# Kernel tuning notes

Measured on AMD Instinct MI355X. Metric: run time of the kernel, lower is better.

The kernel has to match this reference:

```python
import jax, jax.numpy as jnp
import numpy as np

T, B, E, H = 1024, 2, 1024, 16
D = E // H


def setup_inputs() -> dict:
    key = jax.random.key(0)
    ks = jax.random.split(key, 5)
    s = 1.0 / np.sqrt(E)  # xavier_uniform bound ~ sqrt(6/(fan_in+fan_out)); scale suffices for a numeric baseline
    return {
        "query": jax.random.normal(ks[0], (T, B, E), jnp.float32),
        "key_": jax.random.normal(ks[1], (T, B, E), jnp.float32),
        "value": jax.random.normal(ks[2], (T, B, E), jnp.float32),
        "in_proj_weight": jax.random.uniform(ks[3], (3 * E, E), jnp.float32, -s, s),
        "in_proj_bias": jnp.zeros((3 * E,), jnp.float32),
        "out_proj_weight": jax.random.uniform(ks[4], (E, E), jnp.float32, -s, s),
        "out_proj_bias": jnp.zeros((E,), jnp.float32),
    }


def reference(query, key_, value, in_proj_weight, in_proj_bias, out_proj_weight, out_proj_bias):
    # Faithful to CumulativeLinearMultiheadAttentionKV.forward with
    # batch_first=False, is_causal=True, no padding mask, no kv cache.
    Tl, Bl, El = query.shape
    wq, wk, wv = jnp.split(in_proj_weight, 3, axis=0)
    bq, bk, bv = jnp.split(in_proj_bias, 3)
    q = query @ wq.T + bq          # (T, B, E)
    k = key_ @ wk.T + bk
    v = value @ wv.T + bv

    def to_bhtd(x):
        return x.reshape(Tl, Bl, H, D).transpose(1, 2, 0, 3)  # (B, H, T, D)

    q, k, v = to_bhtd(q), to_bhtd(k), to_bhtd(v)

    scale = 1.0 / np.sqrt(D)  # SDPA-style default scale (scale=None)
    # cumulative linear attention: prefix sums of k_s \otimes v_s
    kv = jnp.einsum('bhsk,bhsv->bhskv', k, v)        # (B, H, T, D, D)
    kv_store = jnp.cumsum(kv, axis=2)                # causal KV state per step
    out = jnp.einsum('bhtk,bhtkv->bhtv', q, kv_store) * scale  # (B, H, T, D)

    out = out.transpose(2, 0, 1, 3).reshape(Tl, Bl, El)  # back to (T, B, E)
    out = out @ out_proj_weight.T + out_proj_bias
    return out
```

## Files before the change

### kernel.cpp

```cpp
#include <hip/hip_runtime.h>


#define E_DIM 1024

typedef short bf16x8 __attribute__((ext_vector_type(8)));
typedef float f32x4  __attribute__((ext_vector_type(4)));

__device__ inline unsigned short f2bf(float f) {
    unsigned u = __builtin_bit_cast(unsigned, f);
    u = (u + 0x7FFFu + ((u >> 16) & 1u)) >> 16;
    return (unsigned short)u;
}

__device__ inline void gload_lds16(const void* g, void* l) {
    __builtin_amdgcn_global_load_lds(
        (const __attribute__((address_space(1))) unsigned int*)g,
        (__attribute__((address_space(3))) unsigned int*)l, 16, 0, 0);
}

__device__ inline int swzb(int row, int colbyte) {
    return colbyte ^ ((row & 7) << 4);
}

__global__ __launch_bounds__(256) void k_cast(
    const float* __restrict__ q_in, const float* __restrict__ k_in,
    const float* __restrict__ v_in, const float* __restrict__ w_in,
    const float* __restrict__ w_out, unsigned short* __restrict__ dst)
{
    #pragma unroll
    for (int l = 0; l < 4; ++l) {
        int id8 = blockIdx.x * 256 + threadIdx.x + l * 327680;
        const float* src;
        if (id8 < 262144)        src = q_in  + (size_t)id8 * 8;
        else if (id8 < 524288)   src = k_in  + (size_t)(id8 - 262144) * 8;
        else if (id8 < 786432)   src = v_in  + (size_t)(id8 - 524288) * 8;
        else if (id8 < 1179648)  src = w_in  + (size_t)(id8 - 786432) * 8;
        else                     src = w_out + (size_t)(id8 - 1179648) * 8;
        float4 f0 = *reinterpret_cast<const float4*>(src);
        float4 f1 = *reinterpret_cast<const float4*>(src + 4);
        ushort4 o0, o1;
        o0.x = f2bf(f0.x); o0.y = f2bf(f0.y); o0.z = f2bf(f0.z); o0.w = f2bf(f0.w);
        o1.x = f2bf(f1.x); o1.y = f2bf(f1.y); o1.z = f2bf(f1.z); o1.w = f2bf(f1.w);
        *reinterpret_cast<ushort4*>(dst + (size_t)id8 * 8)     = o0;
        *reinterpret_cast<ushort4*>(dst + (size_t)id8 * 8 + 4) = o1;
    }
}

__global__ __launch_bounds__(256) void k_gin(
    const unsigned short* __restrict__ xbf, const unsigned short* __restrict__ Wibf,
    const float* __restrict__ b_in,
    unsigned short* __restrict__ qslab, unsigned short* __restrict__ kslab,
    unsigned short* __restrict__ ktb,   unsigned short* __restrict__ vtb)
{
    const int i = blockIdx.x;
    const int xcd = i & 7, j = i >> 3;
    const int p = xcd * 12 + (j >> 2);
    const int x = j & 3;
    const int z = p >> 5, y = p & 31;

    const unsigned short* X = xbf + (size_t)z * 2097152;
    const unsigned short* W = Wibf + (size_t)z * 1048576;
    const float* bz = b_in + z * E_DIM;

    const int nBase = x * 256;
    const int mBase = y * 64;
    const int b = mBase >> 10, tBase = mBase & 1023;

    __shared__ short As[2][64 * 64];
    __shared__ short Bs[2][256 * 64];

    const int tid = threadIdx.x;
    const int lane = tid & 63, wave = tid >> 6;
    const int wr = wave >> 1, wc = wave & 1;
    const int l15 = lane & 15, l4 = lane >> 4;

    auto stage = [&](int bufI, int k0) {
        #pragma unroll
        for (int l = 0; l < 8; ++l) {
            int off = l * 4096 + tid * 16;
            int row = off >> 7, cb = off & 127;
            gload_lds16((const char*)W + ((size_t)(nBase + row) * E_DIM + k0) * 2
                            + swzb(row, cb),
                        (char*)&Bs[bufI][0] + off);
        }
        #pragma unroll
        for (int l = 0; l < 2; ++l) {
            int off = l * 4096 + tid * 16;
            int row = off >> 7, cb = off & 127;
            gload_lds16((const char*)X +
                            ((size_t)((tBase + row) * 2 + b) * E_DIM + k0) * 2
                            + swzb(row, cb),
                        (char*)&As[bufI][0] + off);
        }
    };

    f32x4 acc[2][8] = {};

    stage(0, 0);
    __syncthreads();
    int cur = 0;
    for (int it = 0; it < 16; ++it) {
        if (it < 15) stage(cur ^ 1, (it + 1) * 64);
        #pragma unroll
        for (int kk = 0; kk < 64; kk += 32) {
            bf16x8 af[2], bfr[8];
            #pragma unroll
            for (int ii = 0; ii < 2; ++ii) {
                int row = wr * 32 + ii * 16 + l15;
                af[ii] = *reinterpret_cast<const bf16x8*>(
                    &As[cur][row * 64 + (swzb(row, (kk + l4 * 8) * 2) >> 1)]);
            }
            #pragma unroll
            for (int jn = 0; jn < 8; ++jn) {
                int row = wc * 128 + jn * 16 + l15;
                bfr[jn] = *reinterpret_cast<const bf16x8*>(
                    &Bs[cur][row * 64 + (swzb(row, (kk + l4 * 8) * 2) >> 1)]);
            }
            #pragma unroll
            for (int ii = 0; ii < 2; ++ii)
                #pragma unroll
                for (int jn = 0; jn < 8; ++jn)
                    acc[ii][jn] = __builtin_amdgcn_mfma_f32_16x16x32_bf16(
                        af[ii], bfr[jn], acc[ii][jn], 0, 0, 0);
        }
        __syncthreads();
        cur ^= 1;
    }

    #pragma unroll
    for (int ii = 0; ii < 2; ++ii) {
        int t0 = tBase + wr * 32 + ii * 16 + l4 * 4;
        #pragma unroll
        for (int jn = 0; jn < 8; ++jn) {
            int col = nBase + wc * 128 + jn * 16 + l15;
            float bv = bz[col];
            unsigned short v4[4];
            #pragma unroll
            for (int q = 0; q < 4; ++q) v4[q] = f2bf(acc[ii][jn][q] + bv);
            if (z == 0) {
                #pragma unroll
                for (int q = 0; q < 4; ++q)
                    qslab[(size_t)b * 1048576 + (size_t)(t0 + q) * E_DIM + col] = v4[q];
            } else if (z == 1) {
                #pragma unroll
                for (int q = 0; q < 4; ++q)
                    kslab[(size_t)b * 1048576 + (size_t)(t0 + q) * E_DIM + col] = v4[q];
                ushort4 w = {v4[0], v4[1], v4[2], v4[3]};
                *reinterpret_cast<ushort4*>(
                    &ktb[((size_t)b * 1024 + col) * 1024 + t0]) = w;
            } else {
                ushort4 w = {v4[0], v4[1], v4[2], v4[3]};
                *reinterpret_cast<ushort4*>(
                    &vtb[((size_t)b * 1024 + col) * 1024 + t0]) = w;
            }
        }
    }
}

__global__ __launch_bounds__(256) void k_attn(
    const unsigned short* __restrict__ qslab, const unsigned short* __restrict__ kslab,
    const unsigned short* __restrict__ ktb,  const unsigned short* __restrict__ vtb,
    unsigned short* __restrict__ attnbf)
{
    const int i = blockIdx.x;
    const int xcd = i & 7, u = i >> 3;
    const int bh = xcd * 4 + (u >> 4);
    const int qtr = u & 15;
    const int qt = ((u >> 5) & 1) ? (15 - qtr) : qtr;
    const int b = bh >> 4, h = bh & 15;
    const int colb = h * 64, t0q = qt * 64;

    __shared__ short Qs[64 * 64];
    __shared__ short KB[2][64 * 64];
    __shared__ short VB[2][64 * 64];
    __shared__ short Ss[64 * 72];
    __shared__ short PTs[64 * 72];

    const int tid = threadIdx.x;
    const int lane = tid & 63, wave = tid >> 6;
    const int wr = wave >> 1, wc = wave & 1;
    const int l15 = lane & 15, l4 = lane >> 4;

    auto stageP = [&](int bufI, int c) {
        int t0k = c * 64;
        #pragma unroll
        for (int l = 0; l < 2; ++l) {
            int off = l * 4096 + tid * 16;
            int row = off >> 7, cb = off & 127;
            int scb = swzb(row, cb);
            size_t trn = ((size_t)(b * 1024 + colb + row)) * 1024 + t0k;
            gload_lds16((const char*)ktb + trn * 2 + scb, (char*)&KB[bufI][0] + off);
            gload_lds16((const char*)vtb + trn * 2 + scb, (char*)&VB[bufI][0] + off);
        }
    };
    auto stageDiag = [&](int bufI) {
        #pragma unroll
        for (int l = 0; l < 2; ++l) {
            int off = l * 4096 + tid * 16;
            int row = off >> 7, cb = off & 127;
            int scb = swzb(row, cb);
            gload_lds16((const char*)kslab +
                            ((size_t)b * 1048576 + (size_t)(t0q + row) * E_DIM + colb) * 2 + scb,
                        (char*)&KB[bufI][0] + off);
            gload_lds16((const char*)vtb +
                            (((size_t)(b * 1024 + colb + row)) * 1024 + t0q) * 2 + scb,
                        (char*)&VB[bufI][0] + off);
        }
    };

    #pragma unroll
    for (int l = 0; l < 2; ++l) {
        int off = l * 4096 + tid * 16;
        int row = off >> 7, cb = off & 127;
        gload_lds16((const char*)qslab +
                        ((size_t)b * 1048576 + (size_t)(t0q + row) * E_DIM + colb) * 2
                        + swzb(row, cb),
                    (char*)Qs + off);
    }
    if (qt > 0) stageP(0, 0); else stageDiag(0);
    __syncthreads();

    f32x4 pacc[2][2] = {};
    int cur = 0;

    for (int c = 0; c < qt; ++c) {
        if (c + 1 < qt) stageP(cur ^ 1, c + 1); else stageDiag(cur ^ 1);
        #pragma unroll
        for (int kk = 0; kk < 64; kk += 32) {
            bf16x8 af[2], bfr[2];
            #pragma unroll
            for (int ii = 0; ii < 2; ++ii) {
                int row = wr * 32 + ii * 16 + l15;
                af[ii] = *reinterpret_cast<const bf16x8*>(
                    &KB[cur][row * 64 + (swzb(row, (kk + l4 * 8) * 2) >> 1)]);
            }
            #pragma unroll
            for (int jn = 0; jn < 2; ++jn) {
                int row = wc * 32 + jn * 16 + l15;
                bfr[jn] = *reinterpret_cast<const bf16x8*>(
                    &VB[cur][row * 64 + (swzb(row, (kk + l4 * 8) * 2) >> 1)]);
            }
            #pragma unroll
            for (int ii = 0; ii < 2; ++ii)
                #pragma unroll
                for (int jn = 0; jn < 2; ++jn)
                    pacc[ii][jn] = __builtin_amdgcn_mfma_f32_16x16x32_bf16(
                        af[ii], bfr[jn], pacc[ii][jn], 0, 0, 0);
        }
        __syncthreads();
        cur ^= 1;
    }

    f32x4 sacc[2][2] = {};
    #pragma unroll
    for (int kk = 0; kk < 64; kk += 32) {
        bf16x8 af[2], bfr[2];
        #pragma unroll
        for (int ii = 0; ii < 2; ++ii) {
            int row = wr * 32 + ii * 16 + l15;
            af[ii] = *reinterpret_cast<const bf16x8*>(
                &Qs[row * 64 + (swzb(row, (kk + l4 * 8) * 2) >> 1)]);
        }
        #pragma unroll
        for (int jn = 0; jn < 2; ++jn) {
            int row = wc * 32 + jn * 16 + l15;
            bfr[jn] = *reinterpret_cast<const bf16x8*>(
                &KB[cur][row * 64 + (swzb(row, (kk + l4 * 8) * 2) >> 1)]);
        }
        #pragma unroll
        for (int ii = 0; ii < 2; ++ii)
            #pragma unroll
            for (int jn = 0; jn < 2; ++jn)
                sacc[ii][jn] = __builtin_amdgcn_mfma_f32_16x16x32_bf16(
                    af[ii], bfr[jn], sacc[ii][jn], 0, 0, 0);
    }

    #pragma unroll
    for (int ii = 0; ii < 2; ++ii) {
        #pragma unroll
        for (int jn = 0; jn < 2; ++jn) {
            int dv = wc * 32 + jn * 16 + l15;
            int dkb = wr * 32 + ii * 16 + l4 * 4;
            ushort4 pw;
            pw.x = f2bf(pacc[ii][jn][0]); pw.y = f2bf(pacc[ii][jn][1]);
            pw.z = f2bf(pacc[ii][jn][2]); pw.w = f2bf(pacc[ii][jn][3]);
            *reinterpret_cast<ushort4*>(&PTs[dv * 72 + dkb]) = pw;
            int kr = dv;
            #pragma unroll
            for (int q = 0; q < 4; ++q) {
                int qr = dkb + q;
                Ss[qr * 72 + kr] = (kr <= qr) ? (short)f2bf(sacc[ii][jn][q]) : (short)0;
            }
        }
    }
    __syncthreads();

    f32x4 oacc[2][2] = {};
    #pragma unroll
    for (int kk = 0; kk < 64; kk += 32) {
        bf16x8 af[2], bfr[2];
        #pragma unroll
        for (int ii = 0; ii < 2; ++ii)
            af[ii] = *reinterpret_cast<const bf16x8*>(
                        &Ss[(wr * 32 + ii * 16 + l15) * 72 + kk + l4 * 8]);
        #pragma unroll
        for (int jn = 0; jn < 2; ++jn) {
            int row = wc * 32 + jn * 16 + l15;
            bfr[jn] = *reinterpret_cast<const bf16x8*>(
                &VB[cur][row * 64 + (swzb(row, (kk + l4 * 8) * 2) >> 1)]);
        }
        #pragma unroll
        for (int ii = 0; ii < 2; ++ii)
            #pragma unroll
            for (int jn = 0; jn < 2; ++jn)
                oacc[ii][jn] = __builtin_amdgcn_mfma_f32_16x16x32_bf16(
                    af[ii], bfr[jn], oacc[ii][jn], 0, 0, 0);
    }
    #pragma unroll
    for (int kk = 0; kk < 64; kk += 32) {
        bf16x8 af[2], bfr[2];
        #pragma unroll
        for (int ii = 0; ii < 2; ++ii) {
            int row = wr * 32 + ii * 16 + l15;
            af[ii] = *reinterpret_cast<const bf16x8*>(
                &Qs[row * 64 + (swzb(row, (kk + l4 * 8) * 2) >> 1)]);
        }
        #pragma unroll
        for (int jn = 0; jn < 2; ++jn)
            bfr[jn] = *reinterpret_cast<const bf16x8*>(
                        &PTs[(wc * 32 + jn * 16 + l15) * 72 + kk + l4 * 8]);
        #pragma unroll
        for (int ii = 0; ii < 2; ++ii)
            #pragma unroll
            for (int jn = 0; jn < 2; ++jn)
                oacc[ii][jn] = __builtin_amdgcn_mfma_f32_16x16x32_bf16(
                    af[ii], bfr[jn], oacc[ii][jn], 0, 0, 0);
    }

    #pragma unroll
    for (int ii = 0; ii < 2; ++ii) {
        #pragma unroll
        for (int jn = 0; jn < 2; ++jn) {
            int dv = wc * 32 + jn * 16 + l15;
            #pragma unroll
            for (int q = 0; q < 4; ++q) {
                int qr = wr * 32 + ii * 16 + l4 * 4 + q;
                attnbf[(size_t)b * 1048576 + (size_t)(t0q + qr) * E_DIM + colb + dv] =
                    f2bf(oacc[ii][jn][q] * 0.125f);
            }
        }
    }
}

__global__ __launch_bounds__(256) void k_gout(
    const unsigned short* __restrict__ attnbf, const unsigned short* __restrict__ Wobf,
    const float* __restrict__ bias, float* __restrict__ out)
{
    const int i = blockIdx.x;
    const int tile = (i & 7) * 64 + (i >> 3);
    const int x = tile & 15, y = tile >> 4;
    const int nBase = x * 64;
    const int mBase = y * 64;

    __shared__ short As[2][64 * 64];
    __shared__ short Bs[2][64 * 64];

    const int tid = threadIdx.x;
    const int lane = tid & 63, wave = tid >> 6;
    const int wr = wave >> 1, wc = wave & 1;
    const int l15 = lane & 15, l4 = lane >> 4;

    auto stage = [&](int bufI, int k0) {
        #pragma unroll
        for (int l = 0; l < 2; ++l) {
            int off = l * 4096 + tid * 16;
            int row = off >> 7, cb = off & 127;
            int scb = swzb(row, cb);
            gload_lds16((const char*)Wobf + ((size_t)(nBase + row) * E_DIM + k0) * 2 + scb,
                        (char*)&Bs[bufI][0] + off);
            int r = mBase + row, t = r >> 1, bb = r & 1;
            gload_lds16((const char*)attnbf +
                            ((size_t)bb * 1048576 + (size_t)t * E_DIM + k0) * 2 + scb,
                        (char*)&As[bufI][0] + off);
        }
    };

    f32x4 acc[2][2] = {};

    stage(0, 0);
    __syncthreads();
    int cur = 0;
    for (int it = 0; it < 16; ++it) {
        if (it < 15) stage(cur ^ 1, (it + 1) * 64);
        #pragma unroll
        for (int kk = 0; kk < 64; kk += 32) {
            bf16x8 af[2], bfr[2];
            #pragma unroll
            for (int ii = 0; ii < 2; ++ii) {
                int row = wr * 32 + ii * 16 + l15;
                af[ii] = *reinterpret_cast<const bf16x8*>(
                    &As[cur][row * 64 + (swzb(row, (kk + l4 * 8) * 2) >> 1)]);
            }
            #pragma unroll
            for (int jn = 0; jn < 2; ++jn) {
                int row = wc * 32 + jn * 16 + l15;
                bfr[jn] = *reinterpret_cast<const bf16x8*>(
                    &Bs[cur][row * 64 + (swzb(row, (kk + l4 * 8) * 2) >> 1)]);
            }
            #pragma unroll
            for (int ii = 0; ii < 2; ++ii)
                #pragma unroll
                for (int jn = 0; jn < 2; ++jn)
                    acc[ii][jn] = __builtin_amdgcn_mfma_f32_16x16x32_bf16(
                        af[ii], bfr[jn], acc[ii][jn], 0, 0, 0);
        }
        __syncthreads();
        cur ^= 1;
    }

    #pragma unroll
    for (int ii = 0; ii < 2; ++ii) {
        int r0 = mBase + wr * 32 + ii * 16 + l4 * 4;
        #pragma unroll
        for (int jn = 0; jn < 2; ++jn) {
            int col = nBase + wc * 32 + jn * 16 + l15;
            float bv = bias[col];
            #pragma unroll
            for (int q = 0; q < 4; ++q)
                out[(size_t)(r0 + q) * E_DIM + col] = acc[ii][jn][q] + bv;
        }
    }
}

extern "C" void kernel_launch(void* const* d_in, const int* in_sizes, int n_in,
                              void* d_out, int out_size, void* d_ws, size_t ws_size,
                              hipStream_t stream)
{
    const float* q_in  = (const float*)d_in[0];
    const float* k_in  = (const float*)d_in[1];
    const float* v_in  = (const float*)d_in[2];
    const float* w_in  = (const float*)d_in[3];
    const float* b_in  = (const float*)d_in[4];
    const float* w_out = (const float*)d_in[5];
    const float* b_out = (const float*)d_in[6];

    char* w = (char*)d_ws;
    unsigned short* xbf    = (unsigned short*)w;
    unsigned short* Wibf   = (unsigned short*)(w + 12582912);
    unsigned short* Wobf   = (unsigned short*)(w + 18874368);
    unsigned short* qslab  = (unsigned short*)(w + 20971520);
    unsigned short* kslab  = (unsigned short*)(w + 25165824);
    unsigned short* ktb    = (unsigned short*)(w + 29360128);
    unsigned short* vtb    = (unsigned short*)(w + 33554432);
    unsigned short* attnbf = (unsigned short*)(w + 37748736);
    float* outp = (float*)d_out;

    k_cast<<<1280, 256, 0, stream>>>(q_in, k_in, v_in, w_in, w_out, xbf);
    k_gin<<<384, 256, 0, stream>>>(xbf, Wibf, b_in, qslab, kslab, ktb, vtb);
    k_attn<<<512, 256, 0, stream>>>(qslab, kslab, ktb, vtb, attnbf);
    k_gout<<<512, 256, 0, stream>>>(attnbf, Wobf, b_out, outp);
}
```

Before: 145.9 us.

## Use partial vmcnt waits to keep two LDS stages in flight across GEMM and attention loops

Replaces the __syncthreads-based double buffer with a schedule that issues two global-to-LDS stages ahead and waits only for the older one with explicit s_waitcnt vmcnt counts plus raw s_barrier. The next stage is issued right after the post-compute barrier, so loads overlap more of the MFMA work in the input projection, the attention loop and the output projection. This depends on exact vmcnt accounting (10 or 4 outstanding loads). A miscount, for example the Q loads in the attention kernel, could produce races.

```diff
diff --git a/kernel.cpp b/kernel.cpp
--- a/kernel.cpp
+++ b/kernel.cpp
@@ -21,6 +21,10 @@
 __device__ inline int swzb(int row, int colbyte) {
     return colbyte ^ ((row & 7) << 4);
 }
+
+#define WAIT_VM(N) do { \
+    asm volatile("s_waitcnt vmcnt(" #N ")" ::: "memory"); \
+    __builtin_amdgcn_sched_barrier(0); } while (0)
 
 __global__ __launch_bounds__(256) void k_cast(
     const float* __restrict__ q_in, const float* __restrict__ k_in,
@@ -74,7 +78,8 @@
     const int wr = wave >> 1, wc = wave & 1;
     const int l15 = lane & 15, l4 = lane >> 4;
 
-    auto stage = [&](int bufI, int k0) {
+    auto stage = [&](int bufI, int it) {
+        int k0 = it * 64;
         #pragma unroll
         for (int l = 0; l < 8; ++l) {
             int off = l * 4096 + tid * 16;
@@ -97,10 +102,11 @@
     f32x4 acc[2][8] = {};
 
     stage(0, 0);
-    __syncthreads();
-    int cur = 0;
+    stage(1, 1);
     for (int it = 0; it < 16; ++it) {
-        if (it < 15) stage(cur ^ 1, (it + 1) * 64);
+        if (it < 15) WAIT_VM(10); else WAIT_VM(0);
+        __builtin_amdgcn_s_barrier();
+        const int cur = it & 1;
         #pragma unroll
         for (int kk = 0; kk < 64; kk += 32) {
             bf16x8 af[2], bfr[8];
@@ -123,8 +129,9 @@
                     acc[ii][jn] = __builtin_amdgcn_mfma_f32_16x16x32_bf16(
                         af[ii], bfr[jn], acc[ii][jn], 0, 0, 0);
         }
-        __syncthreads();
-        cur ^= 1;
+        __builtin_amdgcn_s_barrier();
+        __builtin_amdgcn_sched_barrier(0);
+        if (it + 2 < 16) stage(cur, it + 2);
     }
 
     #pragma unroll
@@ -181,30 +188,24 @@
     const int wr = wave >> 1, wc = wave & 1;
     const int l15 = lane & 15, l4 = lane >> 4;
 
-    auto stageP = [&](int bufI, int c) {
-        int t0k = c * 64;
+    auto stage = [&](int bufI, int tau) {
         #pragma unroll
         for (int l = 0; l < 2; ++l) {
             int off = l * 4096 + tid * 16;
             int row = off >> 7, cb = off & 127;
             int scb = swzb(row, cb);
-            size_t trn = ((size_t)(b * 1024 + colb + row)) * 1024 + t0k;
-            gload_lds16((const char*)ktb + trn * 2 + scb, (char*)&KB[bufI][0] + off);
-            gload_lds16((const char*)vtb + trn * 2 + scb, (char*)&VB[bufI][0] + off);
-        }
-    };
-    auto stageDiag = [&](int bufI) {
-        #pragma unroll
-        for (int l = 0; l < 2; ++l) {
-            int off = l * 4096 + tid * 16;
-            int row = off >> 7, cb = off & 127;
-            int scb = swzb(row, cb);
-            gload_lds16((const char*)kslab +
-                            ((size_t)b * 1048576 + (size_t)(t0q + row) * E_DIM + colb) * 2 + scb,
-                        (char*)&KB[bufI][0] + off);
-            gload_lds16((const char*)vtb +
-                            (((size_t)(b * 1024 + colb + row)) * 1024 + t0q) * 2 + scb,
-                        (char*)&VB[bufI][0] + off);
+            if (tau < qt) {
+                size_t trn = ((size_t)(b * 1024 + colb + row)) * 1024 + tau * 64;
+                gload_lds16((const char*)ktb + trn * 2 + scb, (char*)&KB[bufI][0] + off);
+                gload_lds16((const char*)vtb + trn * 2 + scb, (char*)&VB[bufI][0] + off);
+            } else {
+                gload_lds16((const char*)kslab +
+                                ((size_t)b * 1048576 + (size_t)(t0q + row) * E_DIM + colb) * 2 + scb,
+                            (char*)&KB[bufI][0] + off);
+                gload_lds16((const char*)vtb +
+                                (((size_t)(b * 1024 + colb + row)) * 1024 + t0q) * 2 + scb,
+                            (char*)&VB[bufI][0] + off);
+            }
         }
     };
 
@@ -217,14 +218,15 @@
                         + swzb(row, cb),
                     (char*)Qs + off);
     }
-    if (qt > 0) stageP(0, 0); else stageDiag(0);
-    __syncthreads();
+    stage(0, 0);
+    if (qt >= 1) stage(1, 1);
 
     f32x4 pacc[2][2] = {};
-    int cur = 0;
-
-    for (int c = 0; c < qt; ++c) {
-        if (c + 1 < qt) stageP(cur ^ 1, c + 1); else stageDiag(cur ^ 1);
+
+    for (int tau = 0; tau < qt; ++tau) {
+        WAIT_VM(4);
+        __builtin_amdgcn_s_barrier();
+        const int cur = tau & 1;
         #pragma unroll
         for (int kk = 0; kk < 64; kk += 32) {
             bf16x8 af[2], bfr[2];
@@ -247,9 +249,14 @@
                     pacc[ii][jn] = __builtin_amdgcn_mfma_f32_16x16x32_bf16(
                         af[ii], bfr[jn], pacc[ii][jn], 0, 0, 0);
         }
-        __syncthreads();
-        cur ^= 1;
-    }
+        __builtin_amdgcn_s_barrier();
+        __builtin_amdgcn_sched_barrier(0);
+        if (tau + 2 <= qt) stage(cur, tau + 2);
+    }
+
+    WAIT_VM(0);
+    __builtin_amdgcn_s_barrier();
+    const int dcur = qt & 1;
 
     f32x4 sacc[2][2] = {};
     #pragma unroll
@@ -265,7 +272,7 @@
         for (int jn = 0; jn < 2; ++jn) {
             int row = wc * 32 + jn * 16 + l15;
             bfr[jn] = *reinterpret_cast<const bf16x8*>(
-                &KB[cur][row * 64 + (swzb(row, (kk + l4 * 8) * 2) >> 1)]);
+                &KB[dcur][row * 64 + (swzb(row, (kk + l4 * 8) * 2) >> 1)]);
         }
         #pragma unroll
         for (int ii = 0; ii < 2; ++ii)
@@ -307,7 +314,7 @@
         for (int jn = 0; jn < 2; ++jn) {
             int row = wc * 32 + jn * 16 + l15;
             bfr[jn] = *reinterpret_cast<const bf16x8*>(
-                &VB[cur][row * 64 + (swzb(row, (kk + l4 * 8) * 2) >> 1)]);
+                &VB[dcur][row * 64 + (swzb(row, (kk + l4 * 8) * 2) >> 1)]);
         }
         #pragma unroll
         for (int ii = 0; ii < 2; ++ii)
@@ -370,7 +377,8 @@
     const int wr = wave >> 1, wc = wave & 1;
     const int l15 = lane & 15, l4 = lane >> 4;
 
-    auto stage = [&](int bufI, int k0) {
+    auto stage = [&](int bufI, int it) {
+        int k0 = it * 64;
         #pragma unroll
         for (int l = 0; l < 2; ++l) {
             int off = l * 4096 + tid * 16;
@@ -388,10 +396,11 @@
     f32x4 acc[2][2] = {};
 
     stage(0, 0);
-    __syncthreads();
-    int cur = 0;
+    stage(1, 1);
     for (int it = 0; it < 16; ++it) {
-        if (it < 15) stage(cur ^ 1, (it + 1) * 64);
+        if (it < 15) WAIT_VM(4); else WAIT_VM(0);
+        __builtin_amdgcn_s_barrier();
+        const int cur = it & 1;
         #pragma unroll
         for (int kk = 0; kk < 64; kk += 32) {
             bf16x8 af[2], bfr[2];
@@ -414,8 +423,9 @@
                     acc[ii][jn] = __builtin_amdgcn_mfma_f32_16x16x32_bf16(
                         af[ii], bfr[jn], acc[ii][jn], 0, 0, 0);
         }
-        __syncthreads();
-        cur ^= 1;
+        __builtin_amdgcn_s_barrier();
+        __builtin_amdgcn_sched_barrier(0);
+        if (it + 2 < 16) stage(cur, it + 2);
     }
 
     #pragma unroll
```

New measurement: 141.9 us. -2.8%, faster.
